# Optimization experiments

Measured on AMD Instinct MI355X. Metric: run time of the kernel, lower is better.

Reference implementation:

```python
import jax, jax.numpy as jnp
import numpy as np

WS = (4, 4, 4)          # window size (s, h, w)
NUM_HEADS = 6
DIM = 192               # kv channels C
CS = 2                  # channel_scale; q/out channels = DIM // CS
B = 256                 # num_windows * batch


def _rel_pos_index(ws):
    """Reproduces the module's relative_position_index buffer (shape [8shw, 2shw])."""
    s, h, w = ws
    cs = np.repeat(np.arange(s), 2)
    ch = np.repeat(np.arange(h), 2)
    cw = np.repeat(np.arange(w), 2)
    coords = np.stack(np.meshgrid(cs, ch, cw, indexing='ij'))   # (3, 2s, 2h, 2w)
    cf = coords.reshape(3, -1)                                   # (3, T), T = 8shw
    rel = cf[:, :, None] - cf[:, None, :]                        # (3, T, T)
    rel = rel[:, :, ::4]                                         # (3, T, T//4)
    rel = np.ascontiguousarray(rel.transpose(1, 2, 0))           # (T, T//4, 3)
    rel[:, :, 0] += s - 1
    rel[:, :, 1] += h - 1
    rel[:, :, 2] += w - 1
    rel[:, :, 0] *= 3 * h - 1
    rel[:, :, 1] *= 2 * h - 1
    return rel.sum(-1).astype(np.int32)                          # (T, T//4)


def setup_inputs() -> dict:
    key = jax.random.key(0)
    ks = jax.random.split(key, 9)
    s, h, w = WS
    qN = 8 * s * h * w          # 512 query tokens per window
    N = qN // 4                 # 128 key/value tokens per window
    C = DIM
    qC = DIM // CS
    table_len = (4 * s - 1) * (4 * h - 1) * (4 * w - 1)
    return {
        'kv': jax.random.normal(ks[0], (B, N, C), jnp.float32),
        'q': jax.random.normal(ks[1], (B, qN, qC), jnp.float32),
        'w_kv': jax.random.normal(ks[2], (C, 2 * C), jnp.float32) * 0.02,
        'b_kv': jnp.zeros((2 * C,), jnp.float32),
        'w_q': jax.random.normal(ks[3], (qC, C), jnp.float32) * 0.02,
        'b_q': jnp.zeros((C,), jnp.float32),
        'w_proj': jax.random.normal(ks[4], (C, qC), jnp.float32) * 0.02,
        'b_proj': jnp.zeros((qC,), jnp.float32),
        'bias_table': jax.random.normal(ks[5], (table_len, NUM_HEADS), jnp.float32) * 0.02,
        'rel_index': jnp.asarray(_rel_pos_index(WS)),
    }


def reference(kv, q, w_kv, b_kv, w_q, b_q, w_proj, b_proj, bias_table, rel_index):
    B_, N, C = kv.shape
    d = C // NUM_HEADS
    scale = d ** -0.5
    # project kv -> k, v : (B_, nH, N, d)
    kvp = (kv @ w_kv + b_kv).reshape(B_, N, 2, NUM_HEADS, d)
    k = kvp[:, :, 0].transpose(0, 2, 1, 3)
    v = kvp[:, :, 1].transpose(0, 2, 1, 3)
    # project q : (B_, nH, qN, d), pre-scaled
    qp = (q @ w_q + b_q).reshape(B_, -1, NUM_HEADS, d).transpose(0, 2, 1, 3) * scale
    attn = jnp.einsum('bhqd,bhkd->bhqk', qp, k)          # (B_, nH, qN, N)
    bias = bias_table[rel_index]                          # (qN, N, nH) gather
    attn = attn + bias.transpose(2, 0, 1)[None]           # + (1, nH, qN, N)
    attn = jax.nn.softmax(attn, axis=-1)
    out = jnp.einsum('bhqk,bhkd->bhqd', attn, v)          # (B_, nH, qN, d)
    out = out.transpose(0, 2, 1, 3).reshape(B_, -1, C)    # (B_, qN, C)
    return out @ w_proj + b_proj                          # (B_, qN, C//CS)
```

## Files before the change

kernel.cpp:

```cpp
#include <hip/hip_runtime.h>
#include <hip/hip_bf16.h>

#define B_    256
#define NKV   128
#define NQ    512
#define CDIM  192
#define QCDIM 96
#define NH    6
#define DH    32
#define SCALE 0.17677669529663687f

typedef __hip_bfloat16 bf16;
typedef __attribute__((ext_vector_type(8))) short s16x8;
typedef __attribute__((ext_vector_type(4))) float f32x4;
#define MFMA16(a, b, c) __builtin_amdgcn_mfma_f32_16x16x32_bf16(a, b, c, 0, 0, 0)

#define OFF_BIASF 0
#define OFF_WKVF  1572864
#define OFF_WQF   1720320
#define OFF_WPF   1757184
#define OFF_KF    1794048
#define OFF_VF    14376960

__global__ __launch_bounds__(256)
void precomp_all(const float* __restrict__ w_kv, const float* __restrict__ w_q,
                 const float* __restrict__ w_proj, const float* __restrict__ bias_table,
                 const int* __restrict__ rel_index,
                 float* __restrict__ biasF, bf16* __restrict__ wkvF,
                 bf16* __restrict__ wqF, bf16* __restrict__ wpF)
{
    const int i = blockIdx.x * 256 + threadIdx.x;
    if (i < 98304) {
        const int lane = i & 63, tl = (i >> 6) & 7, rowblk = (i >> 9) & 31, h = i >> 14;
        const int quad = lane >> 4, l16 = lane & 15;
        const int kvi = tl * 16 + l16;
        float vr[4];
        #pragma unroll
        for (int r = 0; r < 4; ++r) {
            const int qrow = rowblk * 16 + quad * 4 + r;
            vr[r] = bias_table[rel_index[qrow * NKV + kvi] * NH + h];
        }
        *(float4*)&biasF[i * 4] = make_float4(vr[0], vr[1], vr[2], vr[3]);
    } else if (i < 98304 + 73728) {
        const int i1 = i - 98304;
        const int j = i1 & 7, lane = (i1 >> 3) & 63, kk = (i1 >> 9) % 6, nt = i1 / 3072;
        const int quad = lane >> 4, l16 = lane & 15;
        wkvF[i1] = __float2bfloat16(w_kv[(kk * 32 + quad * 8 + j) * (2 * CDIM) + nt * 16 + l16]);
    } else if (i < 98304 + 92160) {
        const int i2 = i - 98304 - 73728;
        const int j = i2 & 7, lane = (i2 >> 3) & 63, kk = (i2 >> 9) % 3,
                  tl = (i2 / 1536) & 1, h = i2 / 3072;
        const int quad = lane >> 4, l16 = lane & 15;
        wqF[i2] = __float2bfloat16(w_q[(kk * 32 + quad * 8 + j) * CDIM + h * DH + tl * 16 + l16] * SCALE);
    } else {
        const int i3 = i - 98304 - 92160;
        const int j = i3 & 7, lane = (i3 >> 3) & 63, tn = (i3 >> 9) % 6, h = i3 / 3072;
        const int quad = lane >> 4, l16 = lane & 15;
        wpF[i3] = __float2bfloat16(w_proj[(h * DH + quad * 8 + j) * QCDIM + tn * 16 + l16]);
    }
}

__global__ __launch_bounds__(512, 4)
void proj_kv(const float* __restrict__ kv, const float* __restrict__ b_kv,
             const bf16* __restrict__ wkvF, bf16* __restrict__ KF, bf16* __restrict__ VF)
{
    __shared__ __align__(16) char smem[52224];
    bf16* sA = (bf16*)smem;
    const int b = blockIdx.x, half = blockIdx.y, t = threadIdx.x;
    const int w = t >> 6, lane = t & 63, quad = lane >> 4, l16 = lane & 15;
    const f32x4 ZV = {0.f, 0.f, 0.f, 0.f};

    for (int f = t; f < 6144; f += 512) {
        const int r = f / 48, c4 = f % 48;
        const float4 v = *(const float4*)&kv[((size_t)b * NKV + r) * CDIM + c4 * 4];
        __align__(8) bf16 tmp[4] = {__float2bfloat16(v.x), __float2bfloat16(v.y),
                                    __float2bfloat16(v.z), __float2bfloat16(v.w)};
        *(uint2*)&sA[r * 200 + c4 * 4] = *(uint2*)tmp;
    }
    __syncthreads();

    f32x4 acc[12];
    #pragma unroll
    for (int i = 0; i < 12; ++i) acc[i] = ZV;
    for (int kk = 0; kk < 6; ++kk) {
        const s16x8 a = *(const s16x8*)&sA[(w * 16 + l16) * 200 + kk * 32 + quad * 8];
        #pragma unroll
        for (int nt = 0; nt < 12; ++nt) {
            const s16x8 bb = *(const s16x8*)&wkvF[(((half * 12 + nt) * 6 + kk) * 64 + lane) * 8];
            acc[nt] = MFMA16(a, bb, acc[nt]);
        }
    }
    __syncthreads();

    if (half == 0) {
        bf16* bufK = (bf16*)smem;
        #pragma unroll
        for (int nt = 0; nt < 12; ++nt) {
            const int col = nt * 16 + l16;
            const float bias = b_kv[col];
            #pragma unroll
            for (int r = 0; r < 4; ++r)
                bufK[(w * 16 + quad * 4 + r) * 200 + col] = __float2bfloat16(acc[nt][r] + bias);
        }
        __syncthreads();
        bf16* KF_b = KF + (size_t)b * 24576;
        #pragma unroll
        for (int i = 0; i < 6; ++i) {
            const int fr = w * 6 + i, h = fr >> 3, tl = fr & 7;
            const s16x8 v = *(const s16x8*)&bufK[(tl * 16 + l16) * 200 + h * DH + quad * 8];
            *(s16x8*)&KF_b[(size_t)(fr * 64 + lane) * 8] = v;
        }
    } else {
        bf16* bufV = (bf16*)smem;
        #pragma unroll
        for (int nt = 0; nt < 12; ++nt) {
            const int d = nt * 16 + l16;
            const float bias = b_kv[CDIM + d];
            __align__(8) bf16 tmp[4];
            #pragma unroll
            for (int r = 0; r < 4; ++r) tmp[r] = __float2bfloat16(acc[nt][r] + bias);
            *(uint2*)&bufV[d * 136 + w * 16 + quad * 4] = *(uint2*)tmp;
        }
        __syncthreads();
        bf16* VF_b = VF + (size_t)b * 24576;
        #pragma unroll
        for (int i = 0; i < 6; ++i) {
            const int fr = w * 6 + i, h = fr >> 3, tl = (fr >> 2) & 1, kk = fr & 3;
            const s16x8 v = *(const s16x8*)&bufV[(h * DH + tl * 16 + l16) * 136 + kk * 32 + quad * 8];
            *(s16x8*)&VF_b[(size_t)(fr * 64 + lane) * 8] = v;
        }
    }
}

__global__ __launch_bounds__(256, 4)
void attn_fused(const float* __restrict__ q, const float* __restrict__ b_q,
                const float* __restrict__ b_proj, const char* __restrict__ wsro,
                float* __restrict__ out)
{
    __shared__ __align__(16) bf16 sP[8 * 16 * 136];
    const int b = blockIdx.x, y = blockIdx.y;
    const int t = threadIdx.x;
    const int w = t >> 6, lane = t & 63, quad = lane >> 4, l16 = lane & 15;
    const f32x4 ZV = {0.f, 0.f, 0.f, 0.f};

    const float* biasF = (const float*)(wsro + OFF_BIASF);
    const bf16*  wqF   = (const bf16*)(wsro + OFF_WQF);
    const bf16*  wpF   = (const bf16*)(wsro + OFF_WPF);
    const bf16*  KF_b  = (const bf16*)(wsro + OFF_KF) + (size_t)b * 24576;
    const bf16*  VF_b  = (const bf16*)(wsro + OFF_VF) + (size_t)b * 24576;

    const int rb[2] = { y * 8 + w, y * 8 + w + 4 };
    bf16* P0 = sP + (2 * w) * 2176;
    bf16* P1 = sP + (2 * w + 1) * 2176;
    bf16* myP[2] = { P0, P1 };

    s16x8 qa[2][3];
    #pragma unroll
    for (int c = 0; c < 2; ++c)
        #pragma unroll
        for (int kk = 0; kk < 3; ++kk) {
            const float* src = &q[((size_t)b * NQ + rb[c] * 16 + l16) * QCDIM + kk * 32 + quad * 8];
            const float4 a0 = *(const float4*)src;
            const float4 a1 = *(const float4*)(src + 4);
            __align__(16) bf16 tmp[8] = {
                __float2bfloat16(a0.x), __float2bfloat16(a0.y), __float2bfloat16(a0.z),
                __float2bfloat16(a0.w), __float2bfloat16(a1.x), __float2bfloat16(a1.y),
                __float2bfloat16(a1.z), __float2bfloat16(a1.w)};
            qa[c][kk] = *(s16x8*)tmp;
        }

    f32x4 outacc[2][6];
    #pragma unroll
    for (int c = 0; c < 2; ++c)
        #pragma unroll
        for (int i = 0; i < 6; ++i) outacc[c][i] = ZV;

    for (int h = 0; h < NH; ++h) {
        #pragma unroll
        for (int c = 0; c < 2; ++c) {
            f32x4 qacc[2];
            qacc[0] = ZV; qacc[1] = ZV;
            #pragma unroll
            for (int kk = 0; kk < 3; ++kk)
                #pragma unroll
                for (int tl = 0; tl < 2; ++tl) {
                    const s16x8 bb = *(const s16x8*)&wqF[(((h * 2 + tl) * 3 + kk) * 64 + lane) * 8];
                    qacc[tl] = MFMA16(qa[c][kk], bb, qacc[tl]);
                }
            #pragma unroll
            for (int tl = 0; tl < 2; ++tl) {
                const float bq = b_q[h * DH + tl * 16 + l16] * SCALE;
                #pragma unroll
                for (int r = 0; r < 4; ++r)
                    myP[c][(quad * 4 + r) * 136 + tl * 16 + l16] = __float2bfloat16(qacc[tl][r] + bq);
            }
            const s16x8 aQ = *(const s16x8*)&myP[c][l16 * 136 + quad * 8];

            float rs[4] = {0.f, 0.f, 0.f, 0.f};
            #pragma unroll
            for (int half = 0; half < 2; ++half) {
                f32x4 sacc[4];
                #pragma unroll
                for (int t4 = 0; t4 < 4; ++t4) {
                    const s16x8 bb = *(const s16x8*)&KF_b[(size_t)((h * 8 + half * 4 + t4) * 64 + lane) * 8];
                    sacc[t4] = MFMA16(aQ, bb, ZV);
                }
                #pragma unroll
                for (int t4 = 0; t4 < 4; ++t4) {
                    const f32x4 b4 = *(const f32x4*)&biasF[(((h * 32 + rb[c]) * 8 + half * 4 + t4) * 64 + lane) * 4];
                    #pragma unroll
                    for (int r = 0; r < 4; ++r) {
                        const float vv = __expf(sacc[t4][r] + b4[r]);
                        rs[r] += vv;
                        myP[c][(quad * 4 + r) * 136 + (half * 4 + t4) * 16 + l16] = __float2bfloat16(vv);
                    }
                }
            }
            float inv[4];
            #pragma unroll
            for (int r = 0; r < 4; ++r) {
                float s = rs[r];
                #pragma unroll
                for (int off = 1; off < 16; off <<= 1) s += __shfl_xor(s, off, 16);
                inv[r] = 1.f / s;
            }

            f32x4 oacc[2];
            oacc[0] = ZV; oacc[1] = ZV;
            #pragma unroll
            for (int kk = 0; kk < 4; ++kk) {
                const s16x8 aP = *(const s16x8*)&myP[c][l16 * 136 + kk * 32 + quad * 8];
                #pragma unroll
                for (int tl = 0; tl < 2; ++tl) {
                    const s16x8 bb = *(const s16x8*)&VF_b[(size_t)(((h * 2 + tl) * 4 + kk) * 64 + lane) * 8];
                    oacc[tl] = MFMA16(aP, bb, oacc[tl]);
                }
            }
            #pragma unroll
            for (int tl = 0; tl < 2; ++tl)
                #pragma unroll
                for (int r = 0; r < 4; ++r)
                    myP[c][(quad * 4 + r) * 136 + tl * 16 + l16] = __float2bfloat16(oacc[tl][r] * inv[r]);

            const s16x8 aO = *(const s16x8*)&myP[c][l16 * 136 + quad * 8];
            #pragma unroll
            for (int tn = 0; tn < 6; ++tn) {
                const s16x8 bb = *(const s16x8*)&wpF[((h * 6 + tn) * 64 + lane) * 8];
                outacc[c][tn] = MFMA16(aO, bb, outacc[c][tn]);
            }
        }
    }

    #pragma unroll
    for (int c = 0; c < 2; ++c)
        #pragma unroll
        for (int tn = 0; tn < 6; ++tn) {
            const float bp = b_proj[tn * 16 + l16];
            #pragma unroll
            for (int r = 0; r < 4; ++r)
                out[((size_t)b * NQ + rb[c] * 16 + quad * 4 + r) * QCDIM + tn * 16 + l16]
                    = outacc[c][tn][r] + bp;
        }
}

extern "C" void kernel_launch(void* const* d_in, const int* in_sizes, int n_in,
                              void* d_out, int out_size, void* d_ws, size_t ws_size,
                              hipStream_t stream)
{
    const float* kv       = (const float*)d_in[0];
    const float* q        = (const float*)d_in[1];
    const float* w_kv     = (const float*)d_in[2];
    const float* b_kv     = (const float*)d_in[3];
    const float* w_q      = (const float*)d_in[4];
    const float* b_q      = (const float*)d_in[5];
    const float* w_proj   = (const float*)d_in[6];
    const float* b_proj   = (const float*)d_in[7];
    const float* bias_tab = (const float*)d_in[8];
    const int*   rel_idx  = (const int*)d_in[9];
    char* ws = (char*)d_ws;

    precomp_all<<<816, 256, 0, stream>>>(w_kv, w_q, w_proj, bias_tab, rel_idx,
                                         (float*)(ws + OFF_BIASF), (bf16*)(ws + OFF_WKVF),
                                         (bf16*)(ws + OFF_WQF), (bf16*)(ws + OFF_WPF));
    proj_kv<<<dim3(B_, 2), 512, 0, stream>>>(kv, b_kv, (const bf16*)(ws + OFF_WKVF),
                                             (bf16*)(ws + OFF_KF), (bf16*)(ws + OFF_VF));
    attn_fused<<<dim3(B_, 4), 256, 0, stream>>>(q, b_q, b_proj, (const char*)ws,
                                                (float*)d_out);
}
```

Before: 228.3 us.

## Interleave two row-chunks per head, share B-fragment loads, fold log2e into exp2

```diff
diff --git a/kernel.cpp b/kernel.cpp
--- a/kernel.cpp
+++ b/kernel.cpp
@@ -9,6 +9,7 @@
 #define NH    6
 #define DH    32
 #define SCALE 0.17677669529663687f
+#define LOG2E 1.4426950408889634f
 
 typedef __hip_bfloat16 bf16;
 typedef __attribute__((ext_vector_type(8))) short s16x8;
@@ -38,7 +39,7 @@
         #pragma unroll
         for (int r = 0; r < 4; ++r) {
             const int qrow = rowblk * 16 + quad * 4 + r;
-            vr[r] = bias_table[rel_index[qrow * NKV + kvi] * NH + h];
+            vr[r] = bias_table[rel_index[qrow * NKV + kvi] * NH + h] * LOG2E;
         }
         *(float4*)&biasF[i * 4] = make_float4(vr[0], vr[1], vr[2], vr[3]);
     } else if (i < 98304 + 73728) {
@@ -51,7 +52,8 @@
         const int j = i2 & 7, lane = (i2 >> 3) & 63, kk = (i2 >> 9) % 3,
                   tl = (i2 / 1536) & 1, h = i2 / 3072;
         const int quad = lane >> 4, l16 = lane & 15;
-        wqF[i2] = __float2bfloat16(w_q[(kk * 32 + quad * 8 + j) * CDIM + h * DH + tl * 16 + l16] * SCALE);
+        wqF[i2] = __float2bfloat16(w_q[(kk * 32 + quad * 8 + j) * CDIM + h * DH + tl * 16 + l16]
+                                   * (SCALE * LOG2E));
     } else {
         const int i3 = i - 98304 - 92160;
         const int j = i3 & 7, lane = (i3 >> 3) & 63, tn = (i3 >> 9) % 6, h = i3 / 3072;
@@ -132,7 +134,7 @@
     }
 }
 
-__global__ __launch_bounds__(256, 4)
+__global__ __launch_bounds__(256, 3)
 void attn_fused(const float* __restrict__ q, const float* __restrict__ b_q,
                 const float* __restrict__ b_proj, const char* __restrict__ wsro,
                 float* __restrict__ out)
@@ -141,7 +143,6 @@
     const int b = blockIdx.x, y = blockIdx.y;
     const int t = threadIdx.x;
     const int w = t >> 6, lane = t & 63, quad = lane >> 4, l16 = lane & 15;
-    const f32x4 ZV = {0.f, 0.f, 0.f, 0.f};
 
     const float* biasF = (const float*)(wsro + OFF_BIASF);
     const bf16*  wqF   = (const bf16*)(wsro + OFF_WQF);
@@ -150,9 +151,7 @@
     const bf16*  VF_b  = (const bf16*)(wsro + OFF_VF) + (size_t)b * 24576;
 
     const int rb[2] = { y * 8 + w, y * 8 + w + 4 };
-    bf16* P0 = sP + (2 * w) * 2176;
-    bf16* P1 = sP + (2 * w + 1) * 2176;
-    bf16* myP[2] = { P0, P1 };
+    bf16* myP[2] = { sP + (2 * w) * 2176, sP + (2 * w + 1) * 2176 };
 
     s16x8 qa[2][3];
     #pragma unroll
@@ -173,94 +172,117 @@
     #pragma unroll
     for (int c = 0; c < 2; ++c)
         #pragma unroll
-        for (int i = 0; i < 6; ++i) outacc[c][i] = ZV;
+        for (int tn = 0; tn < 6; ++tn) {
+            const float bp = b_proj[tn * 16 + l16];
+            outacc[c][tn] = (f32x4){bp, bp, bp, bp};
+        }
 
     for (int h = 0; h < NH; ++h) {
-        #pragma unroll
-        for (int c = 0; c < 2; ++c) {
-            f32x4 qacc[2];
-            qacc[0] = ZV; qacc[1] = ZV;
-            #pragma unroll
-            for (int kk = 0; kk < 3; ++kk)
-                #pragma unroll
-                for (int tl = 0; tl < 2; ++tl) {
-                    const s16x8 bb = *(const s16x8*)&wqF[(((h * 2 + tl) * 3 + kk) * 64 + lane) * 8];
-                    qacc[tl] = MFMA16(qa[c][kk], bb, qacc[tl]);
-                }
+        f32x4 qacc[2][2];
+        #pragma unroll
+        for (int tl = 0; tl < 2; ++tl) {
+            const float bq = b_q[h * DH + tl * 16 + l16] * (SCALE * LOG2E);
+            qacc[0][tl] = (f32x4){bq, bq, bq, bq};
+            qacc[1][tl] = (f32x4){bq, bq, bq, bq};
+        }
+        #pragma unroll
+        for (int kk = 0; kk < 3; ++kk)
             #pragma unroll
             for (int tl = 0; tl < 2; ++tl) {
-                const float bq = b_q[h * DH + tl * 16 + l16] * SCALE;
+                const s16x8 bb = *(const s16x8*)&wqF[(((h * 2 + tl) * 3 + kk) * 64 + lane) * 8];
+                qacc[0][tl] = MFMA16(qa[0][kk], bb, qacc[0][tl]);
+                qacc[1][tl] = MFMA16(qa[1][kk], bb, qacc[1][tl]);
+            }
+        #pragma unroll
+        for (int c = 0; c < 2; ++c)
+            #pragma unroll
+            for (int tl = 0; tl < 2; ++tl)
                 #pragma unroll
                 for (int r = 0; r < 4; ++r)
-                    myP[c][(quad * 4 + r) * 136 + tl * 16 + l16] = __float2bfloat16(qacc[tl][r] + bq);
+                    myP[c][(quad * 4 + r) * 136 + tl * 16 + l16] = __float2bfloat16(qacc[c][tl][r]);
+        s16x8 aQ[2];
+        aQ[0] = *(const s16x8*)&myP[0][l16 * 136 + quad * 8];
+        aQ[1] = *(const s16x8*)&myP[1][l16 * 136 + quad * 8];
+
+        float rs[2][4] = {{0.f, 0.f, 0.f, 0.f}, {0.f, 0.f, 0.f, 0.f}};
+        #pragma unroll
+        for (int half = 0; half < 2; ++half) {
+            f32x4 sacc[2][4];
+            #pragma unroll
+            for (int c = 0; c < 2; ++c)
+                #pragma unroll
+                for (int t4 = 0; t4 < 4; ++t4)
+                    sacc[c][t4] = *(const f32x4*)&biasF[(((h * 32 + rb[c]) * 8 + half * 4 + t4) * 64 + lane) * 4];
+            #pragma unroll
+            for (int t4 = 0; t4 < 4; ++t4) {
+                const s16x8 bb = *(const s16x8*)&KF_b[(size_t)((h * 8 + half * 4 + t4) * 64 + lane) * 8];
+                sacc[0][t4] = MFMA16(aQ[0], bb, sacc[0][t4]);
+                sacc[1][t4] = MFMA16(aQ[1], bb, sacc[1][t4]);
             }
-            const s16x8 aQ = *(const s16x8*)&myP[c][l16 * 136 + quad * 8];
-
-            float rs[4] = {0.f, 0.f, 0.f, 0.f};
-            #pragma unroll
-            for (int half = 0; half < 2; ++half) {
-                f32x4 sacc[4];
-                #pragma unroll
-                for (int t4 = 0; t4 < 4; ++t4) {
-                    const s16x8 bb = *(const s16x8*)&KF_b[(size_t)((h * 8 + half * 4 + t4) * 64 + lane) * 8];
-                    sacc[t4] = MFMA16(aQ, bb, ZV);
-                }
-                #pragma unroll
-                for (int t4 = 0; t4 < 4; ++t4) {
-                    const f32x4 b4 = *(const f32x4*)&biasF[(((h * 32 + rb[c]) * 8 + half * 4 + t4) * 64 + lane) * 4];
+            #pragma unroll
+            for (int c = 0; c < 2; ++c)
+                #pragma unroll
+                for (int t4 = 0; t4 < 4; ++t4)
                     #pragma unroll
                     for (int r = 0; r < 4; ++r) {
-                        const float vv = __expf(sacc[t4][r] + b4[r]);
-                        rs[r] += vv;
+                        const float vv = __builtin_amdgcn_exp2f(sacc[c][t4][r]);
+                        rs[c][r] += vv;
                         myP[c][(quad * 4 + r) * 136 + (half * 4 + t4) * 16 + l16] = __float2bfloat16(vv);
                     }
-                }
+        }
+        float inv[2][4];
+        #pragma unroll
+        for (int c = 0; c < 2; ++c)
+            #pragma unroll
+            for (int r = 0; r < 4; ++r) {
+                float s = rs[c][r];
+                #pragma unroll
+                for (int off = 1; off < 16; off <<= 1) s += __shfl_xor(s, off, 16);
+                inv[c][r] = 1.f / s;
             }
-            float inv[4];
-            #pragma unroll
-            for (int r = 0; r < 4; ++r) {
-                float s = rs[r];
-                #pragma unroll
-                for (int off = 1; off < 16; off <<= 1) s += __shfl_xor(s, off, 16);
-                inv[r] = 1.f / s;
+
+        f32x4 oacc[2][2];
+        oacc[0][0] = (f32x4){0.f, 0.f, 0.f, 0.f}; oacc[0][1] = (f32x4){0.f, 0.f, 0.f, 0.f};
+        oacc[1][0] = (f32x4){0.f, 0.f, 0.f, 0.f}; oacc[1][1] = (f32x4){0.f, 0.f, 0.f, 0.f};
+        #pragma unroll
+        for (int kk = 0; kk < 4; ++kk) {
+            s16x8 aP[2];
+            aP[0] = *(const s16x8*)&myP[0][l16 * 136 + kk * 32 + quad * 8];
+            aP[1] = *(const s16x8*)&myP[1][l16 * 136 + kk * 32 + quad * 8];
+            #pragma unroll
+            for (int tl = 0; tl < 2; ++tl) {
+                const s16x8 bb = *(const s16x8*)&VF_b[(size_t)(((h * 2 + tl) * 4 + kk) * 64 + lane) * 8];
+                oacc[0][tl] = MFMA16(aP[0], bb, oacc[0][tl]);
+                oacc[1][tl] = MFMA16(aP[1], bb, oacc[1][tl]);
             }
-
-            f32x4 oacc[2];
-            oacc[0] = ZV; oacc[1] = ZV;
-            #pragma unroll
-            for (int kk = 0; kk < 4; ++kk) {
-                const s16x8 aP = *(const s16x8*)&myP[c][l16 * 136 + kk * 32 + quad * 8];
-                #pragma unroll
-                for (int tl = 0; tl < 2; ++tl) {
-                    const s16x8 bb = *(const s16x8*)&VF_b[(size_t)(((h * 2 + tl) * 4 + kk) * 64 + lane) * 8];
-                    oacc[tl] = MFMA16(aP, bb, oacc[tl]);
-                }
-            }
+        }
+        #pragma unroll
+        for (int c = 0; c < 2; ++c)
             #pragma unroll
             for (int tl = 0; tl < 2; ++tl)
                 #pragma unroll
                 for (int r = 0; r < 4; ++r)
-                    myP[c][(quad * 4 + r) * 136 + tl * 16 + l16] = __float2bfloat16(oacc[tl][r] * inv[r]);
-
-            const s16x8 aO = *(const s16x8*)&myP[c][l16 * 136 + quad * 8];
-            #pragma unroll
-            for (int tn = 0; tn < 6; ++tn) {
-                const s16x8 bb = *(const s16x8*)&wpF[((h * 6 + tn) * 64 + lane) * 8];
-                outacc[c][tn] = MFMA16(aO, bb, outacc[c][tn]);
-            }
+                    myP[c][(quad * 4 + r) * 136 + tl * 16 + l16] = __float2bfloat16(oacc[c][tl][r] * inv[c][r]);
+        s16x8 aO[2];
+        aO[0] = *(const s16x8*)&myP[0][l16 * 136 + quad * 8];
+        aO[1] = *(const s16x8*)&myP[1][l16 * 136 + quad * 8];
+
+        #pragma unroll
+        for (int tn = 0; tn < 6; ++tn) {
+            const s16x8 bb = *(const s16x8*)&wpF[((h * 6 + tn) * 64 + lane) * 8];
+            outacc[0][tn] = MFMA16(aO[0], bb, outacc[0][tn]);
+            outacc[1][tn] = MFMA16(aO[1], bb, outacc[1][tn]);
         }
     }
 
     #pragma unroll
     for (int c = 0; c < 2; ++c)
         #pragma unroll
-        for (int tn = 0; tn < 6; ++tn) {
-            const float bp = b_proj[tn * 16 + l16];
+        for (int tn = 0; tn < 6; ++tn)
             #pragma unroll
             for (int r = 0; r < 4; ++r)
                 out[((size_t)b * NQ + rb[c] * 16 + quad * 4 + r) * QCDIM + tn * 16 + l16]
-                    = outacc[c][tn][r] + bp;
-        }
+                    = outacc[c][tn][r];
 }
 
 extern "C" void kernel_launch(void* const* d_in, const int* in_sizes, int n_in,
```

After: 256.3 us. 1.12x slower.
